# Kernel optimization log

Hardware: AMD Instinct MI355X
Metric: run time of the kernel (lower is better)

Reference implementation:

```python
import jax, jax.numpy as jnp
import numpy as np

B, D, P = 1024, 1024, 16  # batch, latent_dim(=out_dim), part_dim

def setup_inputs() -> dict:
    key = jax.random.key(0)
    k1, k2 = jax.random.split(key)
    x = jax.random.normal(k1, (B, D, P), dtype=jnp.float32)
    # per-part Linear weights, torch Linear weight shape [out, in] stacked over parts
    W = jax.random.normal(k2, (P, D, D), dtype=jnp.float32) * 0.02
    return {"x": x, "W": W}

def reference(x, W):
    # x: [B, D, P]; W: [P, O, D] (O == D here). stack_dim=-1: slice last dim,
    # apply part-specific Linear (no bias) + exact GELU, stack on last dim.
    y = jnp.einsum('bdp,pod->bop', x, W)  # grouped per-part GEMM -> [B, O, P]
    return jax.nn.gelu(y, approximate=False)
```

## Files before the change

### kernel.cpp

```cpp
#include <hip/hip_runtime.h>
#include <hip/hip_bf16.h>
#include <math.h>

typedef __hip_bfloat16 bf16;
typedef __attribute__((ext_vector_type(8))) short bf16x8;
typedef __attribute__((ext_vector_type(4))) float f32x4;
typedef __attribute__((ext_vector_type(16))) float f32x16;

#define DI static __device__ __forceinline__

constexpr int NB = 1024;
constexpr int ND = 1024;
constexpr int NP = 16;
constexpr int BKT = 32;
constexpr int NKT = ND / BKT;

DI float gelu_exact(float x) {
    return 0.5f * x * (1.0f + erff(x * 0.70710678118654752f));
}

DI ushort bf16_bits(float f) {
    bf16 h = __float2bfloat16(f);
    return *reinterpret_cast<ushort*>(&h);
}

__global__ __launch_bounds__(256) void pack_kernel(const float* __restrict__ x,
                                                   const float* __restrict__ w,
                                                   bf16* __restrict__ xp,
                                                   bf16* __restrict__ wp) {
    __shared__ ushort lds[16][268];
    const int t = threadIdx.x;
    if (blockIdx.x < 4096) {
        const int b = blockIdx.x >> 2;
        const int q = blockIdx.x & 3;
        const float* xb = x + ((size_t)b * ND + q * 256) * NP;
        float4 va[2], vb[2];
#pragma unroll
        for (int it = 0; it < 2; ++it) {
            const int u  = it * 256 + t;
            const int dh = u >> 2;
            const int p0 = (u & 3) * 4;
            va[it] = *reinterpret_cast<const float4*>(&xb[(size_t)(dh * 2)     * NP + p0]);
            vb[it] = *reinterpret_cast<const float4*>(&xb[(size_t)(dh * 2 + 1) * NP + p0]);
        }
        __builtin_amdgcn_sched_barrier(0);
#pragma unroll
        for (int it = 0; it < 2; ++it) {
            const int u  = it * 256 + t;
            const int dh = u >> 2;
            const int p0 = (u & 3) * 4;
            const float a0[4] = { va[it].x, va[it].y, va[it].z, va[it].w };
            const float a1[4] = { vb[it].x, vb[it].y, vb[it].z, vb[it].w };
#pragma unroll
            for (int k = 0; k < 4; ++k) {
                const uint packed = (uint)bf16_bits(a0[k]) | ((uint)bf16_bits(a1[k]) << 16);
                *reinterpret_cast<uint*>(&lds[p0 + k][dh * 2]) = packed;
            }
        }
        __syncthreads();
        const int p = t >> 4, j = t & 15;
        bf16* dst = xp + (size_t)p * (NB * ND) + (size_t)b * ND + q * 256;
#pragma unroll
        for (int it = 0; it < 2; ++it) {
            const int c = it * 16 + j;
            *reinterpret_cast<bf16x8*>(&dst[c * 8]) =
                *reinterpret_cast<const bf16x8*>(&lds[p][c * 8]);
        }
    } else {
        const size_t base = (size_t)(blockIdx.x - 4096) * 4096;
        float4 f[4];
#pragma unroll
        for (int k = 0; k < 4; ++k)
            f[k] = *reinterpret_cast<const float4*>(&w[base + (size_t)k * 1024 + t * 4]);
        __builtin_amdgcn_sched_barrier(0);
#pragma unroll
        for (int k = 0; k < 4; ++k) {
            alignas(8) bf16 tmp[4] = { __float2bfloat16(f[k].x), __float2bfloat16(f[k].y),
                                       __float2bfloat16(f[k].z), __float2bfloat16(f[k].w) };
            *reinterpret_cast<uint2*>(&wp[base + (size_t)k * 1024 + t * 4]) =
                *reinterpret_cast<const uint2*>(tmp);
        }
    }
}

__global__ __launch_bounds__(512, 2) void gemm8_kernel(const bf16* __restrict__ xp,
                                                       const bf16* __restrict__ wp,
                                                       bf16* __restrict__ y) {
    __shared__ bf16 As[3][256 * BKT];
    __shared__ bf16 Bs[3][256 * BKT];
    const int i = blockIdx.x;
    const int p    = ((i & 7) << 1) | ((i >> 3) & 1);
    const int tile = i >> 4;
    const int bt = (tile >> 2) * 256;
    const int ot = (tile & 3) * 256;
    const bf16* A  = xp + (size_t)p * NB * ND;
    const bf16* Bm = wp + (size_t)p * ND * ND;
    const int t = threadIdx.x;
    const int l = t & 63, w = t >> 6;
    const int wr = w >> 2, wc = w & 3;
    const int lr32 = l & 31, g2 = l >> 5;

    f32x16 acc[4][2] = {};

    auto stage = [&](int buf, int kt, int q) {
        const int s   = ((q & 1) * 8 + w) * 64 + l;
        const int row = s >> 2;
        const int cb  = (s & 3) ^ ((row >> 1) & 3);
        const bf16* gsrc = (q < 2 ? A + (size_t)(bt + row) * ND
                                  : Bm + (size_t)(ot + row) * ND) + kt * BKT + cb * 8;
        bf16* ldst = (q < 2 ? &As[buf][((q & 1) * 8 + w) * 512]
                            : &Bs[buf][((q & 1) * 8 + w) * 512]);
        __builtin_amdgcn_global_load_lds((const __attribute__((address_space(1))) void*)gsrc,
                                         (__attribute__((address_space(3))) void*)ldst, 16, 0, 0);
    };
    auto readA = [&](int buf, int m, int s) -> bf16x8 {
        const int row  = wr * 128 + m * 32 + lr32;
        const int ch   = s * 2 + g2;
        const int slot = row * 4 + (ch ^ ((row >> 1) & 3));
        return *reinterpret_cast<const bf16x8*>(&As[buf][slot * 8]);
    };
    auto readB = [&](int buf, int n, int s) -> bf16x8 {
        const int row  = wc * 64 + n * 32 + lr32;
        const int ch   = s * 2 + g2;
        const int slot = row * 4 + (ch ^ ((row >> 1) & 3));
        return *reinterpret_cast<const bf16x8*>(&Bs[buf][slot * 8]);
    };

#pragma unroll
    for (int q = 0; q < 4; ++q) stage(0, 0, q);
#pragma unroll
    for (int q = 0; q < 4; ++q) stage(1, 1, q);
    asm volatile("s_waitcnt vmcnt(4)" ::: "memory");
    __builtin_amdgcn_s_barrier();
    __builtin_amdgcn_sched_barrier(0);

    int bufc = 0, bufs = 2;
#pragma unroll 1
    for (int kt = 0; kt < NKT; ++kt) {
        bf16x8 bfr[2], af[4];
#pragma unroll
        for (int n = 0; n < 2; ++n) bfr[n] = readB(bufc, n, 0);
#pragma unroll
        for (int m = 0; m < 4; ++m) af[m] = readA(bufc, m, 0);
        if (kt + 2 < NKT) { stage(bufs, kt + 2, 0); stage(bufs, kt + 2, 1); }
        __builtin_amdgcn_s_barrier();
        asm volatile("s_waitcnt lgkmcnt(0)" ::: "memory");
        __builtin_amdgcn_s_setprio(1);
#pragma unroll
        for (int m = 0; m < 4; ++m)
#pragma unroll
            for (int n = 0; n < 2; ++n)
                acc[m][n] = __builtin_amdgcn_mfma_f32_32x32x16_bf16(af[m], bfr[n], acc[m][n], 0, 0, 0);
        __builtin_amdgcn_s_setprio(0);
        __builtin_amdgcn_s_barrier();
#pragma unroll
        for (int n = 0; n < 2; ++n) bfr[n] = readB(bufc, n, 1);
#pragma unroll
        for (int m = 0; m < 4; ++m) af[m] = readA(bufc, m, 1);
        if (kt + 2 < NKT) { stage(bufs, kt + 2, 2); stage(bufs, kt + 2, 3); }
        __builtin_amdgcn_s_barrier();
        asm volatile("s_waitcnt lgkmcnt(0)" ::: "memory");
        __builtin_amdgcn_s_setprio(1);
#pragma unroll
        for (int m = 0; m < 4; ++m)
#pragma unroll
            for (int n = 0; n < 2; ++n)
                acc[m][n] = __builtin_amdgcn_mfma_f32_32x32x16_bf16(af[m], bfr[n], acc[m][n], 0, 0, 0);
        __builtin_amdgcn_s_setprio(0);
        if (kt < NKT - 1) {
            if (kt + 2 < NKT) asm volatile("s_waitcnt vmcnt(4)" ::: "memory");
            else              asm volatile("s_waitcnt vmcnt(0)" ::: "memory");
            __builtin_amdgcn_s_barrier();
            __builtin_amdgcn_sched_barrier(0);
        }
        bufc = (bufc == 2) ? 0 : bufc + 1;
        bufs = (bufs == 2) ? 0 : bufs + 1;
    }

    bf16* yp = y + (size_t)p * NB * ND;
#pragma unroll
    for (int m = 0; m < 4; ++m) {
#pragma unroll
        for (int n = 0; n < 2; ++n) {
#pragma unroll
            for (int reg = 0; reg < 16; ++reg) {
                const int row = bt + wr * 128 + m * 32 + (reg & 3) + 8 * (reg >> 2) + 4 * g2;
                const int col = ot + wc * 64 + n * 32 + lr32;
                yp[(size_t)row * ND + col] = __float2bfloat16(acc[m][n][reg]);
            }
        }
    }
}

__global__ __launch_bounds__(256) void unpack_kernel(const bf16* __restrict__ y,
                                                     float* __restrict__ out) {
    const size_t gidx = (size_t)blockIdx.x * 256 + threadIdx.x;
    const size_t o = gidx & 1023;
    const size_t b = gidx >> 10;
    const bf16* yb = y + b * (size_t)ND + o;
    float v[16];
#pragma unroll
    for (int p = 0; p < 16; ++p)
        v[p] = gelu_exact(__bfloat162float(yb[(size_t)p * (NB * ND)]));
    float4* dst = reinterpret_cast<float4*>(out + gidx * NP);
#pragma unroll
    for (int q = 0; q < 4; ++q)
        dst[q] = make_float4(v[q * 4], v[q * 4 + 1], v[q * 4 + 2], v[q * 4 + 3]);
}

__global__ __launch_bounds__(256) void fallback_kernel(const float* __restrict__ x,
                                                       const float* __restrict__ w,
                                                       float* __restrict__ out) {
    __shared__ float As[64][17];
    __shared__ float Bs[64][17];
    const int p = blockIdx.z, bt = blockIdx.y * 64, ot = blockIdx.x * 64;
    const int t = threadIdx.x;
    const int tx = t & 15, ty = t >> 4;
    float acc[4][4] = {};
    for (int k0 = 0; k0 < ND; k0 += 16) {
        __syncthreads();
#pragma unroll
        for (int i = 0; i < 4; ++i) {
            const int idx = i * 256 + t;
            const int r = idx >> 4, k = idx & 15;
            As[r][k] = x[((size_t)(bt + r) * ND + k0 + k) * NP + p];
            Bs[r][k] = w[(size_t)p * ND * ND + (size_t)(ot + r) * ND + k0 + k];
        }
        __syncthreads();
#pragma unroll
        for (int k = 0; k < 16; ++k) {
            float a[4], bb[4];
#pragma unroll
            for (int i = 0; i < 4; ++i) a[i] = As[ty * 4 + i][k];
#pragma unroll
            for (int j = 0; j < 4; ++j) bb[j] = Bs[tx * 4 + j][k];
#pragma unroll
            for (int i = 0; i < 4; ++i)
#pragma unroll
                for (int j = 0; j < 4; ++j) acc[i][j] += a[i] * bb[j];
        }
    }
#pragma unroll
    for (int i = 0; i < 4; ++i)
#pragma unroll
        for (int j = 0; j < 4; ++j)
            out[((size_t)(bt + ty * 4 + i) * ND + (ot + tx * 4 + j)) * NP + p] =
                gelu_exact(acc[i][j]);
}

extern "C" void kernel_launch(void* const* d_in, const int* in_sizes, int n_in,
                              void* d_out, int out_size, void* d_ws, size_t ws_size,
                              hipStream_t stream) {
    const float* x = (const float*)d_in[0];
    const float* w = (const float*)d_in[1];
    float* out = (float*)d_out;

    const size_t nElem     = (size_t)NP * NB * ND;
    const size_t packBytes = nElem * sizeof(bf16) * 2;
    const size_t yBytes    = nElem * sizeof(bf16);

    if (ws_size >= packBytes + yBytes) {
        bf16* xp = (bf16*)d_ws;
        bf16* wp = xp + nElem;
        bf16* y  = (bf16*)((char*)d_ws + packBytes);
        pack_kernel<<<8192, 256, 0, stream>>>(x, w, xp, wp);
        gemm8_kernel<<<256, 512, 0, stream>>>(xp, wp, y);
        unpack_kernel<<<(int)(NB * ND / 256), 256, 0, stream>>>(y, out);
    } else {
        fallback_kernel<<<dim3(16, 16, 16), 256, 0, stream>>>(x, w, out);
    }
}
```

Measured before the change: 112.1 us.

## Load A fragments directly into registers, keep only B in LDS

The GEMM kernel stops staging the A tile through shared memory. Each wave now loads its A MFMA fragments straight from global memory into two register sets that alternate across an unrolled-by-two k loop, while B still goes through a triple-buffered LDS path with global_load_lds. This removes half the LDS traffic and the extra barriers around the A reads. In exchange it uses more VGPRs, so occupancy drops to one block per CU. It also relies on uncoalesced, row-strided 16-byte global loads for A, with a larger vmcnt window to hide their latency.

```diff
diff --git a/kernel.cpp b/kernel.cpp
--- a/kernel.cpp
+++ b/kernel.cpp
@@ -83,10 +83,9 @@
     }
 }
 
-__global__ __launch_bounds__(512, 2) void gemm8_kernel(const bf16* __restrict__ xp,
+__global__ __launch_bounds__(512, 1) void gemm8_kernel(const bf16* __restrict__ xp,
                                                        const bf16* __restrict__ wp,
                                                        bf16* __restrict__ y) {
-    __shared__ bf16 As[3][256 * BKT];
     __shared__ bf16 Bs[3][256 * BKT];
     const int i = blockIdx.x;
     const int p    = ((i & 7) << 1) | ((i >> 3) & 1);
@@ -101,23 +100,27 @@
     const int lr32 = l & 31, g2 = l >> 5;
 
     f32x16 acc[4][2] = {};
-
-    auto stage = [&](int buf, int kt, int q) {
-        const int s   = ((q & 1) * 8 + w) * 64 + l;
-        const int row = s >> 2;
-        const int cb  = (s & 3) ^ ((row >> 1) & 3);
-        const bf16* gsrc = (q < 2 ? A + (size_t)(bt + row) * ND
-                                  : Bm + (size_t)(ot + row) * ND) + kt * BKT + cb * 8;
-        bf16* ldst = (q < 2 ? &As[buf][((q & 1) * 8 + w) * 512]
-                            : &Bs[buf][((q & 1) * 8 + w) * 512]);
-        __builtin_amdgcn_global_load_lds((const __attribute__((address_space(1))) void*)gsrc,
-                                         (__attribute__((address_space(3))) void*)ldst, 16, 0, 0);
+    bf16x8 aA[8], aB[8];
+
+    auto stageB = [&](int buf, int kt) {
+#pragma unroll
+        for (int q = 0; q < 2; ++q) {
+            const int s   = (q * 8 + w) * 64 + l;
+            const int row = s >> 2;
+            const int cb  = (s & 3) ^ ((row >> 1) & 3);
+            const bf16* gsrc = Bm + (size_t)(ot + row) * ND + kt * BKT + cb * 8;
+            bf16* ldst = &Bs[buf][(q * 8 + w) * 512];
+            __builtin_amdgcn_global_load_lds((const __attribute__((address_space(1))) void*)gsrc,
+                                             (__attribute__((address_space(3))) void*)ldst, 16, 0, 0);
+        }
     };
-    auto readA = [&](int buf, int m, int s) -> bf16x8 {
-        const int row  = wr * 128 + m * 32 + lr32;
-        const int ch   = s * 2 + g2;
-        const int slot = row * 4 + (ch ^ ((row >> 1) & 3));
-        return *reinterpret_cast<const bf16x8*>(&As[buf][slot * 8]);
+    auto loadA = [&](int kt, bf16x8 (&r)[8]) {
+#pragma unroll
+        for (int m = 0; m < 4; ++m)
+#pragma unroll
+            for (int s = 0; s < 2; ++s)
+                r[m * 2 + s] = *reinterpret_cast<const bf16x8*>(
+                    &A[(size_t)(bt + wr * 128 + m * 32 + lr32) * ND + kt * BKT + (s * 2 + g2) * 8]);
     };
     auto readB = [&](int buf, int n, int s) -> bf16x8 {
         const int row  = wc * 64 + n * 32 + lr32;
@@ -126,56 +129,47 @@
         return *reinterpret_cast<const bf16x8*>(&Bs[buf][slot * 8]);
     };
 
-#pragma unroll
-    for (int q = 0; q < 4; ++q) stage(0, 0, q);
-#pragma unroll
-    for (int q = 0; q < 4; ++q) stage(1, 1, q);
-    asm volatile("s_waitcnt vmcnt(4)" ::: "memory");
+#define GEMM_BODY(K, AR)                                                              \
+    {                                                                                 \
+        const int c_ = (K) % 3;                                                       \
+        bf16x8 bfr[2];                                                                \
+        bfr[0] = readB(c_, 0, 0); bfr[1] = readB(c_, 1, 0);                           \
+        __builtin_amdgcn_s_setprio(1);                                                \
+        _Pragma("unroll")                                                             \
+        for (int m = 0; m < 4; ++m) {                                                 \
+            acc[m][0] = __builtin_amdgcn_mfma_f32_32x32x16_bf16(AR[m*2], bfr[0], acc[m][0], 0, 0, 0); \
+            acc[m][1] = __builtin_amdgcn_mfma_f32_32x32x16_bf16(AR[m*2], bfr[1], acc[m][1], 0, 0, 0); \
+        }                                                                             \
+        __builtin_amdgcn_s_setprio(0);                                                \
+        bfr[0] = readB(c_, 0, 1); bfr[1] = readB(c_, 1, 1);                           \
+        __builtin_amdgcn_s_setprio(1);                                                \
+        _Pragma("unroll")                                                             \
+        for (int m = 0; m < 4; ++m) {                                                 \
+            acc[m][0] = __builtin_amdgcn_mfma_f32_32x32x16_bf16(AR[m*2+1], bfr[0], acc[m][0], 0, 0, 0); \
+            acc[m][1] = __builtin_amdgcn_mfma_f32_32x32x16_bf16(AR[m*2+1], bfr[1], acc[m][1], 0, 0, 0); \
+        }                                                                             \
+        __builtin_amdgcn_s_setprio(0);                                                \
+        if ((K) + 2 < NKT) { loadA((K) + 2, AR); stageB(((K) + 2) % 3, (K) + 2); }    \
+        if ((K) + 1 < NKT) {                                                          \
+            if ((K) + 2 < NKT) asm volatile("s_waitcnt vmcnt(10)" ::: "memory");      \
+            else               asm volatile("s_waitcnt vmcnt(0)"  ::: "memory");      \
+            __builtin_amdgcn_s_barrier();                                             \
+            __builtin_amdgcn_sched_barrier(0);                                        \
+        }                                                                             \
+    }
+
+    loadA(0, aA); stageB(0, 0);
+    loadA(1, aB); stageB(1, 1);
+    asm volatile("s_waitcnt vmcnt(10)" ::: "memory");
     __builtin_amdgcn_s_barrier();
     __builtin_amdgcn_sched_barrier(0);
 
-    int bufc = 0, bufs = 2;
 #pragma unroll 1
-    for (int kt = 0; kt < NKT; ++kt) {
-        bf16x8 bfr[2], af[4];
-#pragma unroll
-        for (int n = 0; n < 2; ++n) bfr[n] = readB(bufc, n, 0);
-#pragma unroll
-        for (int m = 0; m < 4; ++m) af[m] = readA(bufc, m, 0);
-        if (kt + 2 < NKT) { stage(bufs, kt + 2, 0); stage(bufs, kt + 2, 1); }
-        __builtin_amdgcn_s_barrier();
-        asm volatile("s_waitcnt lgkmcnt(0)" ::: "memory");
-        __builtin_amdgcn_s_setprio(1);
-#pragma unroll
-        for (int m = 0; m < 4; ++m)
-#pragma unroll
-            for (int n = 0; n < 2; ++n)
-                acc[m][n] = __builtin_amdgcn_mfma_f32_32x32x16_bf16(af[m], bfr[n], acc[m][n], 0, 0, 0);
-        __builtin_amdgcn_s_setprio(0);
-        __builtin_amdgcn_s_barrier();
-#pragma unroll
-        for (int n = 0; n < 2; ++n) bfr[n] = readB(bufc, n, 1);
-#pragma unroll
-        for (int m = 0; m < 4; ++m) af[m] = readA(bufc, m, 1);
-        if (kt + 2 < NKT) { stage(bufs, kt + 2, 2); stage(bufs, kt + 2, 3); }
-        __builtin_amdgcn_s_barrier();
-        asm volatile("s_waitcnt lgkmcnt(0)" ::: "memory");
-        __builtin_amdgcn_s_setprio(1);
-#pragma unroll
-        for (int m = 0; m < 4; ++m)
-#pragma unroll
-            for (int n = 0; n < 2; ++n)
-                acc[m][n] = __builtin_amdgcn_mfma_f32_32x32x16_bf16(af[m], bfr[n], acc[m][n], 0, 0, 0);
-        __builtin_amdgcn_s_setprio(0);
-        if (kt < NKT - 1) {
-            if (kt + 2 < NKT) asm volatile("s_waitcnt vmcnt(4)" ::: "memory");
-            else              asm volatile("s_waitcnt vmcnt(0)" ::: "memory");
-            __builtin_amdgcn_s_barrier();
-            __builtin_amdgcn_sched_barrier(0);
-        }
-        bufc = (bufc == 2) ? 0 : bufc + 1;
-        bufs = (bufs == 2) ? 0 : bufs + 1;
-    }
+    for (int kt = 0; kt < NKT; kt += 2) {
+        GEMM_BODY(kt, aA);
+        GEMM_BODY(kt + 1, aB);
+    }
+#undef GEMM_BODY
 
     bf16* yp = y + (size_t)p * NB * ND;
 #pragma unroll
```

After: 141.7 us. 1.26x slower.

## Fuse GELU epilogue into GEMM and drop the intermediate bf16 buffer

Applied to the files above, without the earlier changes.

The GEMM now applies exact GELU to its fp32 accumulators and writes directly into the interleaved [B, O, P] fp32 output. This removes the bf16 intermediate buffer and the separate unpack kernel, avoiding a full write and re-read of the GEMM result and cutting one launch. The cost is that each output store is a 4-byte write at a 64-byte stride, so stores are poorly coalesced, and each output line is assembled from partial writes by blocks for different parts. The pack kernel is also split into separate x and W kernels, and the block-to-part mapping changes, which moves how same-part tiles are spread across XCDs.

```diff
diff --git a/kernel.cpp b/kernel.cpp
--- a/kernel.cpp
+++ b/kernel.cpp
@@ -24,73 +24,73 @@
     return *reinterpret_cast<ushort*>(&h);
 }
 
-__global__ __launch_bounds__(256) void pack_kernel(const float* __restrict__ x,
-                                                   const float* __restrict__ w,
-                                                   bf16* __restrict__ xp,
-                                                   bf16* __restrict__ wp) {
+__global__ __launch_bounds__(256) void pack_x_kernel(const float* __restrict__ x,
+                                                     bf16* __restrict__ xp) {
     __shared__ ushort lds[16][268];
     const int t = threadIdx.x;
-    if (blockIdx.x < 4096) {
-        const int b = blockIdx.x >> 2;
-        const int q = blockIdx.x & 3;
-        const float* xb = x + ((size_t)b * ND + q * 256) * NP;
-        float4 va[2], vb[2];
-#pragma unroll
-        for (int it = 0; it < 2; ++it) {
-            const int u  = it * 256 + t;
-            const int dh = u >> 2;
-            const int p0 = (u & 3) * 4;
-            va[it] = *reinterpret_cast<const float4*>(&xb[(size_t)(dh * 2)     * NP + p0]);
-            vb[it] = *reinterpret_cast<const float4*>(&xb[(size_t)(dh * 2 + 1) * NP + p0]);
-        }
-        __builtin_amdgcn_sched_barrier(0);
-#pragma unroll
-        for (int it = 0; it < 2; ++it) {
-            const int u  = it * 256 + t;
-            const int dh = u >> 2;
-            const int p0 = (u & 3) * 4;
-            const float a0[4] = { va[it].x, va[it].y, va[it].z, va[it].w };
-            const float a1[4] = { vb[it].x, vb[it].y, vb[it].z, vb[it].w };
-#pragma unroll
-            for (int k = 0; k < 4; ++k) {
-                const uint packed = (uint)bf16_bits(a0[k]) | ((uint)bf16_bits(a1[k]) << 16);
-                *reinterpret_cast<uint*>(&lds[p0 + k][dh * 2]) = packed;
-            }
-        }
-        __syncthreads();
-        const int p = t >> 4, j = t & 15;
-        bf16* dst = xp + (size_t)p * (NB * ND) + (size_t)b * ND + q * 256;
-#pragma unroll
-        for (int it = 0; it < 2; ++it) {
-            const int c = it * 16 + j;
-            *reinterpret_cast<bf16x8*>(&dst[c * 8]) =
-                *reinterpret_cast<const bf16x8*>(&lds[p][c * 8]);
-        }
-    } else {
-        const size_t base = (size_t)(blockIdx.x - 4096) * 4096;
-        float4 f[4];
-#pragma unroll
-        for (int k = 0; k < 4; ++k)
-            f[k] = *reinterpret_cast<const float4*>(&w[base + (size_t)k * 1024 + t * 4]);
-        __builtin_amdgcn_sched_barrier(0);
+    const int b = blockIdx.x >> 2;
+    const int q = blockIdx.x & 3;
+    const float* xb = x + ((size_t)b * ND + q * 256) * NP;
+    float4 va[2], vb[2];
+#pragma unroll
+    for (int it = 0; it < 2; ++it) {
+        const int u  = it * 256 + t;
+        const int dh = u >> 2;
+        const int p0 = (u & 3) * 4;
+        va[it] = *reinterpret_cast<const float4*>(&xb[(size_t)(dh * 2)     * NP + p0]);
+        vb[it] = *reinterpret_cast<const float4*>(&xb[(size_t)(dh * 2 + 1) * NP + p0]);
+    }
+    __builtin_amdgcn_sched_barrier(0);
+#pragma unroll
+    for (int it = 0; it < 2; ++it) {
+        const int u  = it * 256 + t;
+        const int dh = u >> 2;
+        const int p0 = (u & 3) * 4;
+        const float a0[4] = { va[it].x, va[it].y, va[it].z, va[it].w };
+        const float a1[4] = { vb[it].x, vb[it].y, vb[it].z, vb[it].w };
 #pragma unroll
         for (int k = 0; k < 4; ++k) {
-            alignas(8) bf16 tmp[4] = { __float2bfloat16(f[k].x), __float2bfloat16(f[k].y),
-                                       __float2bfloat16(f[k].z), __float2bfloat16(f[k].w) };
-            *reinterpret_cast<uint2*>(&wp[base + (size_t)k * 1024 + t * 4]) =
-                *reinterpret_cast<const uint2*>(tmp);
-        }
+            const uint packed = (uint)bf16_bits(a0[k]) | ((uint)bf16_bits(a1[k]) << 16);
+            *reinterpret_cast<uint*>(&lds[p0 + k][dh * 2]) = packed;
+        }
+    }
+    __syncthreads();
+    const int p = t >> 4, j = t & 15;
+    bf16* dst = xp + (size_t)p * (NB * ND) + (size_t)b * ND + q * 256;
+#pragma unroll
+    for (int it = 0; it < 2; ++it) {
+        const int c = it * 16 + j;
+        *reinterpret_cast<bf16x8*>(&dst[c * 8]) =
+            *reinterpret_cast<const bf16x8*>(&lds[p][c * 8]);
+    }
+}
+
+__global__ __launch_bounds__(256) void pack_w_kernel(const float* __restrict__ w,
+                                                     bf16* __restrict__ wp) {
+    const int t = threadIdx.x;
+    const size_t base = (size_t)blockIdx.x * 4096;
+    float4 f[4];
+#pragma unroll
+    for (int k = 0; k < 4; ++k)
+        f[k] = *reinterpret_cast<const float4*>(&w[base + (size_t)k * 1024 + t * 4]);
+    __builtin_amdgcn_sched_barrier(0);
+#pragma unroll
+    for (int k = 0; k < 4; ++k) {
+        alignas(8) bf16 tmp[4] = { __float2bfloat16(f[k].x), __float2bfloat16(f[k].y),
+                                   __float2bfloat16(f[k].z), __float2bfloat16(f[k].w) };
+        *reinterpret_cast<uint2*>(&wp[base + (size_t)k * 1024 + t * 4]) =
+            *reinterpret_cast<const uint2*>(tmp);
     }
 }
 
 __global__ __launch_bounds__(512, 2) void gemm8_kernel(const bf16* __restrict__ xp,
                                                        const bf16* __restrict__ wp,
-                                                       bf16* __restrict__ y) {
+                                                       float* __restrict__ out) {
     __shared__ bf16 As[3][256 * BKT];
     __shared__ bf16 Bs[3][256 * BKT];
     const int i = blockIdx.x;
-    const int p    = ((i & 7) << 1) | ((i >> 3) & 1);
-    const int tile = i >> 4;
+    const int p    = i >> 4;
+    const int tile = i & 15;
     const int bt = (tile >> 2) * 256;
     const int ot = (tile & 3) * 256;
     const bf16* A  = xp + (size_t)p * NB * ND;
@@ -177,7 +177,6 @@
         bufs = (bufs == 2) ? 0 : bufs + 1;
     }
 
-    bf16* yp = y + (size_t)p * NB * ND;
 #pragma unroll
     for (int m = 0; m < 4; ++m) {
 #pragma unroll
@@ -186,26 +185,10 @@
             for (int reg = 0; reg < 16; ++reg) {
                 const int row = bt + wr * 128 + m * 32 + (reg & 3) + 8 * (reg >> 2) + 4 * g2;
                 const int col = ot + wc * 64 + n * 32 + lr32;
-                yp[(size_t)row * ND + col] = __float2bfloat16(acc[m][n][reg]);
+                out[((size_t)row * ND + col) * NP + p] = gelu_exact(acc[m][n][reg]);
             }
         }
     }
-}
-
-__global__ __launch_bounds__(256) void unpack_kernel(const bf16* __restrict__ y,
-                                                     float* __restrict__ out) {
-    const size_t gidx = (size_t)blockIdx.x * 256 + threadIdx.x;
-    const size_t o = gidx & 1023;
-    const size_t b = gidx >> 10;
-    const bf16* yb = y + b * (size_t)ND + o;
-    float v[16];
-#pragma unroll
-    for (int p = 0; p < 16; ++p)
-        v[p] = gelu_exact(__bfloat162float(yb[(size_t)p * (NB * ND)]));
-    float4* dst = reinterpret_cast<float4*>(out + gidx * NP);
-#pragma unroll
-    for (int q = 0; q < 4; ++q)
-        dst[q] = make_float4(v[q * 4], v[q * 4 + 1], v[q * 4 + 2], v[q * 4 + 3]);
 }
 
 __global__ __launch_bounds__(256) void fallback_kernel(const float* __restrict__ x,
@@ -257,15 +240,13 @@
 
     const size_t nElem     = (size_t)NP * NB * ND;
     const size_t packBytes = nElem * sizeof(bf16) * 2;
-    const size_t yBytes    = nElem * sizeof(bf16);
-
-    if (ws_size >= packBytes + yBytes) {
+
+    if (ws_size >= packBytes) {
         bf16* xp = (bf16*)d_ws;
         bf16* wp = xp + nElem;
-        bf16* y  = (bf16*)((char*)d_ws + packBytes);
-        pack_kernel<<<8192, 256, 0, stream>>>(x, w, xp, wp);
-        gemm8_kernel<<<256, 512, 0, stream>>>(xp, wp, y);
-        unpack_kernel<<<(int)(NB * ND / 256), 256, 0, stream>>>(y, out);
+        pack_x_kernel<<<4096, 256, 0, stream>>>(x, xp);
+        pack_w_kernel<<<4096, 256, 0, stream>>>(w, wp);
+        gemm8_kernel<<<256, 512, 0, stream>>>(xp, wp, out);
     } else {
         fallback_kernel<<<dim3(16, 16, 16), 256, 0, stream>>>(x, w, out);
     }
```

New measurement: 145.7 us. 1.3x slower.
